# Kernel optimization log

Measured on AMD Instinct MI355X. Metric: run time of the kernel, lower is better.

Reference implementation:

```python
import jax, jax.numpy as jnp
import numpy as np

B, S, T, D = 32, 128, 65536, 768
VOCAB, N_SEC, N_TEMP, N_NEG, MAX_SENT, N_TS = 30522, 6, 3, 2, 128, 512
LN_EPS = 1e-5


def setup_inputs() -> dict:
    key = jax.random.key(0)
    ks = jax.random.split(key, 16)
    return {
        "token_ids": jax.random.randint(ks[0], (T,), 0, VOCAB),
        "segment_ids": jnp.sort(jax.random.randint(ks[1], (T,), 0, B * S)),
        "section_ids": jax.random.randint(ks[2], (B, S), 0, N_SEC),
        "temporality_ids": jax.random.randint(ks[3], (B, S), 0, N_TEMP),
        "negation_ids": jax.random.randint(ks[4], (B, S), 0, N_NEG),
        "position_ids": jax.random.randint(ks[5], (B, S), 0, MAX_SENT),
        "timestamp_ids": jax.random.randint(ks[6], (B, S), 0, N_TS),
        "token_table": jax.random.normal(ks[7], (VOCAB, D), jnp.float32),
        "section_table": jax.random.normal(ks[8], (N_SEC, D), jnp.float32),
        "temporality_table": jax.random.normal(ks[9], (N_TEMP, D), jnp.float32),
        "negation_table": jax.random.normal(ks[10], (N_NEG, D), jnp.float32),
        "position_table": jax.random.normal(ks[11], (MAX_SENT, D), jnp.float32),
        "timestamp_table": jax.random.normal(ks[12], (N_TS, D), jnp.float32),
        "ln_gamma": jnp.ones((D,), jnp.float32),
        "ln_beta": jnp.zeros((D,), jnp.float32),
        "proj_w": jax.random.normal(ks[13], (D, D), jnp.float32) * (1.0 / np.sqrt(D)),
        "proj_b": jnp.zeros((D,), jnp.float32),
    }


def reference(token_ids, segment_ids, section_ids, temporality_ids, negation_ids,
              position_ids, timestamp_ids, token_table, section_table,
              temporality_table, negation_table, position_table, timestamp_table,
              ln_gamma, ln_beta, proj_w, proj_b):
    # ragged per-sentence token-embedding mean pool (segment mean over B*S slots)
    tok = token_table[token_ids]                                  # [T, D]
    sums = jax.ops.segment_sum(tok, segment_ids, num_segments=B * S)
    cnt = jax.ops.segment_sum(jnp.ones((T,), tok.dtype), segment_ids,
                              num_segments=B * S)
    base = (sums / jnp.maximum(cnt, 1.0)[:, None]).reshape(B, S, D)
    # multi-embedding sum
    enriched = (base
                + section_table[section_ids]
                + temporality_table[temporality_ids]
                + negation_table[negation_ids]
                + position_table[position_ids]
                + timestamp_table[timestamp_ids])                 # [B, S, D]
    # LayerNorm + Linear
    mu = enriched.mean(-1, keepdims=True)
    var = jnp.mean(jnp.square(enriched - mu), axis=-1, keepdims=True)
    normed = (enriched - mu) * jax.lax.rsqrt(var + LN_EPS) * ln_gamma + ln_beta
    tokens = jnp.einsum('bsd,ed->bse', normed, proj_w) + proj_b   # [B, S, D]
    padding_mask = jnp.zeros((B, S), dtype=bool)                  # all sentences valid
    return tokens, padding_mask
```

## Files before the change

kernel.cpp:

```cpp
#include <hip/hip_runtime.h>
#include <stdint.h>

#define Tn 65536
#define Dn 768
#define NSEG 4096

typedef __bf16 bf16;
typedef __bf16 bf16x8 __attribute__((ext_vector_type(8)));
typedef float f32x4 __attribute__((ext_vector_type(4)));

__device__ inline void f4add(float4& a, const float4& v) {
  a.x += v.x; a.y += v.y; a.z += v.z; a.w += v.w;
}

__global__ __launch_bounds__(256) void k_prep(
    const float* __restrict__ w, bf16* __restrict__ wb,
    float* __restrict__ mask_out,
    const int* __restrict__ seg, int* __restrict__ starts)
{
  const int b = blockIdx.x;
  if (b < 576) {
    const int i = b * 256 + threadIdx.x;
    const float4 v = ((const float4*)w)[i];
    alignas(8) bf16 o[4] = {(bf16)v.x, (bf16)v.y, (bf16)v.z, (bf16)v.w};
    ((ushort4*)wb)[i] = *(ushort4*)o;
  } else if (b < 592) {
    mask_out[(b - 576) * 256 + threadIdx.x] = 0.0f;
  } else {
    const int t = (b - 592) * 256 + threadIdx.x;
    const int s = seg[t];
    const int sp = (t == 0) ? -1 : seg[t - 1];
    for (int k = sp + 1; k <= s; ++k) starts[k] = t;
    if (t == Tn - 1)
      for (int k = s + 1; k <= NSEG; ++k) starts[k] = Tn;
  }
}

__global__ void k_pool_ln(
    const int* __restrict__ token_ids, const int* __restrict__ starts,
    const int* __restrict__ section_ids, const int* __restrict__ temporality_ids,
    const int* __restrict__ negation_ids, const int* __restrict__ position_ids,
    const int* __restrict__ timestamp_ids,
    const float* __restrict__ token_table, const float* __restrict__ section_table,
    const float* __restrict__ temporality_table, const float* __restrict__ negation_table,
    const float* __restrict__ position_table, const float* __restrict__ timestamp_table,
    const float* __restrict__ gamma, const float* __restrict__ beta,
    bf16* __restrict__ out_normed)
{
  const int n = blockIdx.x;
  const int lane = threadIdx.x;
  const int start = starts[n];
  const int end   = starts[n + 1];
  const float scale = 1.0f / fmaxf((float)(end - start), 1.0f);

  const float4* tt = (const float4*)token_table;

  const float4* e1 = (const float4*)(section_table     + (size_t)section_ids[n]     * Dn);
  const float4* e2 = (const float4*)(temporality_table + (size_t)temporality_ids[n] * Dn);
  const float4* e3 = (const float4*)(negation_table    + (size_t)negation_ids[n]    * Dn);
  const float4* e4 = (const float4*)(position_table    + (size_t)position_ids[n]    * Dn);
  const float4* e5 = (const float4*)(timestamp_table   + (size_t)timestamp_ids[n]   * Dn);
  float4 en[3];
  #pragma unroll
  for (int j = 0; j < 3; ++j) {
    const int d = j * 64 + lane;
    float4 q = e1[d];
    f4add(q, e2[d]); f4add(q, e3[d]); f4add(q, e4[d]); f4add(q, e5[d]);
    en[j] = q;
  }

  float4 acc[3];
  #pragma unroll
  for (int j = 0; j < 3; ++j) acc[j] = make_float4(0.f, 0.f, 0.f, 0.f);

  int t = start;
  int ids[8];
  #pragma unroll
  for (int u = 0; u < 8; ++u)
    ids[u] = token_ids[(t + u < Tn) ? t + u : Tn - 1];

  while (t + 8 <= end) {
    float4 L[8][3];
    #pragma unroll
    for (int u = 0; u < 8; ++u) {
      const float4* r = tt + (size_t)ids[u] * 192;
      #pragma unroll
      for (int j = 0; j < 3; ++j) L[u][j] = r[j * 64 + lane];
    }
    t += 8;
    #pragma unroll
    for (int u = 0; u < 8; ++u)
      ids[u] = token_ids[(t + u < Tn) ? t + u : Tn - 1];
    #pragma unroll
    for (int j = 0; j < 3; ++j) {
      f4add(L[0][j], L[1][j]); f4add(L[2][j], L[3][j]);
      f4add(L[4][j], L[5][j]); f4add(L[6][j], L[7][j]);
      f4add(L[0][j], L[2][j]); f4add(L[4][j], L[6][j]);
      f4add(L[0][j], L[4][j]); f4add(acc[j], L[0][j]);
    }
  }
  for (int u = 0; t < end; ++t, ++u) {
    const float4* r = tt + (size_t)ids[u] * 192;
    #pragma unroll
    for (int j = 0; j < 3; ++j) f4add(acc[j], r[j * 64 + lane]);
  }

  float4 e[3];
  #pragma unroll
  for (int j = 0; j < 3; ++j) {
    e[j].x = acc[j].x * scale + en[j].x;
    e[j].y = acc[j].y * scale + en[j].y;
    e[j].z = acc[j].z * scale + en[j].z;
    e[j].w = acc[j].w * scale + en[j].w;
  }

  float s = 0.f;
  #pragma unroll
  for (int j = 0; j < 3; ++j) s += e[j].x + e[j].y + e[j].z + e[j].w;
  #pragma unroll
  for (int o = 32; o > 0; o >>= 1) s += __shfl_xor(s, o, 64);
  const float mu = s * (1.0f / 768.0f);

  float v = 0.f;
  #pragma unroll
  for (int j = 0; j < 3; ++j) {
    e[j].x -= mu; e[j].y -= mu; e[j].z -= mu; e[j].w -= mu;
    v += e[j].x * e[j].x + e[j].y * e[j].y + e[j].z * e[j].z + e[j].w * e[j].w;
  }
  #pragma unroll
  for (int o = 32; o > 0; o >>= 1) v += __shfl_xor(v, o, 64);
  const float inv = rsqrtf(v * (1.0f / 768.0f) + 1e-5f);

  #pragma unroll
  for (int j = 0; j < 3; ++j) {
    const int d = j * 64 + lane;
    const float4 g = ((const float4*)gamma)[d];
    const float4 b = ((const float4*)beta)[d];
    alignas(8) bf16 o[4];
    o[0] = (bf16)(e[j].x * inv * g.x + b.x);
    o[1] = (bf16)(e[j].y * inv * g.y + b.y);
    o[2] = (bf16)(e[j].z * inv * g.z + b.z);
    o[3] = (bf16)(e[j].w * inv * g.w + b.w);
    *(ushort4*)(out_normed + (size_t)n * Dn + 4 * d) = *(ushort4*)o;
  }
}

__global__ __launch_bounds__(256) void k_gemm(
    const bf16* __restrict__ A, const bf16* __restrict__ W,
    const float* __restrict__ bias, float* __restrict__ out)
{
  __shared__ bf16 As[64 * 32];
  __shared__ bf16 Bs[128 * 32];
  const int tid  = threadIdx.x;
  const int lane = tid & 63;
  const int w    = tid >> 6;
  const int m0 = blockIdx.y * 64;
  const int n0 = blockIdx.x * 128;
  const int wm = (w >> 1) * 32;
  const int wn = (w & 1) * 64;

  f32x4 acc[2][4];
  #pragma unroll
  for (int i = 0; i < 2; ++i)
    #pragma unroll
    for (int j = 0; j < 4; ++j) acc[i][j] = (f32x4){0.f, 0.f, 0.f, 0.f};

  const int fr = tid >> 2;
  const int fc = (tid & 3) * 8;
  const bf16* agp = A + (size_t)(m0 + fr) * 768 + fc;
  const bf16* bgp = W + (size_t)(n0 + fr) * 768 + fc;

  for (int kt = 0; kt < 24; ++kt) {
    __syncthreads();
    __builtin_amdgcn_global_load_lds(
        (const __attribute__((address_space(1))) void*)(agp + kt * 32),
        (__attribute__((address_space(3))) void*)(As + tid * 8), 16, 0, 0);
    #pragma unroll
    for (int it = 0; it < 2; ++it) {
      const int f = it * 256 + tid;
      __builtin_amdgcn_global_load_lds(
          (const __attribute__((address_space(1))) void*)(bgp + (size_t)it * 64 * 768 + kt * 32),
          (__attribute__((address_space(3))) void*)(Bs + f * 8), 16, 0, 0);
    }
    __syncthreads();

    bf16x8 af[2], bfr[4];
    #pragma unroll
    for (int i = 0; i < 2; ++i)
      af[i] = *(const bf16x8*)(As + (wm + i * 16 + (lane & 15)) * 32 + (lane >> 4) * 8);
    #pragma unroll
    for (int j = 0; j < 4; ++j)
      bfr[j] = *(const bf16x8*)(Bs + (wn + j * 16 + (lane & 15)) * 32 + (lane >> 4) * 8);

    #pragma unroll
    for (int i = 0; i < 2; ++i)
      #pragma unroll
      for (int j = 0; j < 4; ++j)
        acc[i][j] = __builtin_amdgcn_mfma_f32_16x16x32_bf16(af[i], bfr[j], acc[i][j], 0, 0, 0);
  }

  float bvals[4];
  #pragma unroll
  for (int j = 0; j < 4; ++j) bvals[j] = bias[n0 + wn + j * 16 + (lane & 15)];
  const int r0 = (lane >> 4) * 4;
  #pragma unroll
  for (int i = 0; i < 2; ++i) {
    #pragma unroll
    for (int r = 0; r < 4; ++r) {
      const int gm = m0 + wm + i * 16 + r0 + r;
      float* orow = out + (size_t)gm * 768 + n0 + wn;
      #pragma unroll
      for (int j = 0; j < 4; ++j)
        orow[j * 16 + (lane & 15)] = acc[i][j][r] + bvals[j];
    }
  }
}

extern "C" void kernel_launch(void* const* d_in, const int* in_sizes, int n_in,
                              void* d_out, int out_size, void* d_ws, size_t ws_size,
                              hipStream_t stream) {
  const int* token_ids       = (const int*)d_in[0];
  const int* segment_ids     = (const int*)d_in[1];
  const int* section_ids     = (const int*)d_in[2];
  const int* temporality_ids = (const int*)d_in[3];
  const int* negation_ids    = (const int*)d_in[4];
  const int* position_ids    = (const int*)d_in[5];
  const int* timestamp_ids   = (const int*)d_in[6];
  const float* token_table       = (const float*)d_in[7];
  const float* section_table     = (const float*)d_in[8];
  const float* temporality_table = (const float*)d_in[9];
  const float* negation_table    = (const float*)d_in[10];
  const float* position_table    = (const float*)d_in[11];
  const float* timestamp_table   = (const float*)d_in[12];
  const float* ln_gamma = (const float*)d_in[13];
  const float* ln_beta  = (const float*)d_in[14];
  const float* proj_w   = (const float*)d_in[15];
  const float* proj_b   = (const float*)d_in[16];

  float* out = (float*)d_out;
  bf16* wsW = (bf16*)d_ws;
  bf16* wsN = wsW + (size_t)Dn * Dn;
  int*  wsS = (int*)((char*)d_ws + (size_t)(Dn * Dn + NSEG * Dn) * 2);

  k_prep<<<848, 256, 0, stream>>>(proj_w, wsW, out + (size_t)NSEG * Dn,
                                  segment_ids, wsS);
  k_pool_ln<<<NSEG, 64, 0, stream>>>(token_ids, wsS, section_ids,
      temporality_ids, negation_ids, position_ids, timestamp_ids,
      token_table, section_table, temporality_table, negation_table,
      position_table, timestamp_table, ln_gamma, ln_beta, wsN);
  k_gemm<<<dim3(6, 64), 256, 0, stream>>>(wsN, wsW, proj_b, out);
}
```

Before: 202.8 us.

## Fuse prep into pooling kernel using per-segment binary search for bounds

Removes the separate prep kernel by folding the weight bf16 conversion and mask zeroing into extra blocks of the pooling kernel. Each segment block now finds its start and end with a 16-step binary search over segment_ids instead of reading a precomputed starts array. Token-row gathers use nontemporal loads, and the unroll drops from 8 to 6 with a launch-bounds occupancy hint. This saves a kernel launch and its dependency, at the cost of extra serialized global reads per block for the search.

```diff
diff --git a/kernel.cpp b/kernel.cpp
--- a/kernel.cpp
+++ b/kernel.cpp
@@ -9,35 +9,12 @@
 typedef __bf16 bf16x8 __attribute__((ext_vector_type(8)));
 typedef float f32x4 __attribute__((ext_vector_type(4)));
 
-__device__ inline void f4add(float4& a, const float4& v) {
-  a.x += v.x; a.y += v.y; a.z += v.z; a.w += v.w;
-}
-
-__global__ __launch_bounds__(256) void k_prep(
-    const float* __restrict__ w, bf16* __restrict__ wb,
-    float* __restrict__ mask_out,
-    const int* __restrict__ seg, int* __restrict__ starts)
-{
-  const int b = blockIdx.x;
-  if (b < 576) {
-    const int i = b * 256 + threadIdx.x;
-    const float4 v = ((const float4*)w)[i];
-    alignas(8) bf16 o[4] = {(bf16)v.x, (bf16)v.y, (bf16)v.z, (bf16)v.w};
-    ((ushort4*)wb)[i] = *(ushort4*)o;
-  } else if (b < 592) {
-    mask_out[(b - 576) * 256 + threadIdx.x] = 0.0f;
-  } else {
-    const int t = (b - 592) * 256 + threadIdx.x;
-    const int s = seg[t];
-    const int sp = (t == 0) ? -1 : seg[t - 1];
-    for (int k = sp + 1; k <= s; ++k) starts[k] = t;
-    if (t == Tn - 1)
-      for (int k = s + 1; k <= NSEG; ++k) starts[k] = Tn;
-  }
-}
-
-__global__ void k_pool_ln(
-    const int* __restrict__ token_ids, const int* __restrict__ starts,
+__device__ inline f32x4 ntload(const f32x4* p) {
+  return __builtin_nontemporal_load(p);
+}
+
+__global__ __launch_bounds__(64, 4) void k_fused(
+    const int* __restrict__ token_ids, const int* __restrict__ seg,
     const int* __restrict__ section_ids, const int* __restrict__ temporality_ids,
     const int* __restrict__ negation_ids, const int* __restrict__ position_ids,
     const int* __restrict__ timestamp_ids,
@@ -45,78 +22,98 @@
     const float* __restrict__ temporality_table, const float* __restrict__ negation_table,
     const float* __restrict__ position_table, const float* __restrict__ timestamp_table,
     const float* __restrict__ gamma, const float* __restrict__ beta,
-    bf16* __restrict__ out_normed)
+    bf16* __restrict__ out_normed,
+    const float* __restrict__ w, bf16* __restrict__ wb,
+    float* __restrict__ mask_out)
 {
-  const int n = blockIdx.x;
+  const int b = blockIdx.x;
   const int lane = threadIdx.x;
-  const int start = starts[n];
-  const int end   = starts[n + 1];
+
+  if (b >= NSEG) {
+    if (b < NSEG + 2304) {
+      const int i = (b - NSEG) * 64 + lane;
+      const float4 v = ((const float4*)w)[i];
+      alignas(8) bf16 o[4] = {(bf16)v.x, (bf16)v.y, (bf16)v.z, (bf16)v.w};
+      ((ushort4*)wb)[i] = *(ushort4*)o;
+    } else {
+      const int i = (b - (NSEG + 2304)) * 64 + lane;
+      ((float4*)mask_out)[i] = make_float4(0.f, 0.f, 0.f, 0.f);
+    }
+    return;
+  }
+
+  const int n = b;
+  int lo1 = 0, hi1 = Tn, lo2 = 0, hi2 = Tn;
+  #pragma unroll 1
+  for (int it = 0; it < 16; ++it) {
+    const int m1 = (lo1 + hi1) >> 1;
+    const int m2 = (lo2 + hi2) >> 1;
+    const int v1 = seg[m1];
+    const int v2 = seg[m2];
+    if (v1 < n)     lo1 = m1 + 1; else hi1 = m1;
+    if (v2 < n + 1) lo2 = m2 + 1; else hi2 = m2;
+  }
+  const int start = lo1, end = lo2;
   const float scale = 1.0f / fmaxf((float)(end - start), 1.0f);
 
-  const float4* tt = (const float4*)token_table;
-
-  const float4* e1 = (const float4*)(section_table     + (size_t)section_ids[n]     * Dn);
-  const float4* e2 = (const float4*)(temporality_table + (size_t)temporality_ids[n] * Dn);
-  const float4* e3 = (const float4*)(negation_table    + (size_t)negation_ids[n]    * Dn);
-  const float4* e4 = (const float4*)(position_table    + (size_t)position_ids[n]    * Dn);
-  const float4* e5 = (const float4*)(timestamp_table   + (size_t)timestamp_ids[n]   * Dn);
-  float4 en[3];
+  const f32x4* tt = (const f32x4*)token_table;
+
+  const f32x4* e1 = (const f32x4*)(section_table     + (size_t)section_ids[n]     * Dn);
+  const f32x4* e2 = (const f32x4*)(temporality_table + (size_t)temporality_ids[n] * Dn);
+  const f32x4* e3 = (const f32x4*)(negation_table    + (size_t)negation_ids[n]    * Dn);
+  const f32x4* e4 = (const f32x4*)(position_table    + (size_t)position_ids[n]    * Dn);
+  const f32x4* e5 = (const f32x4*)(timestamp_table   + (size_t)timestamp_ids[n]   * Dn);
+  f32x4 en[3];
   #pragma unroll
   for (int j = 0; j < 3; ++j) {
     const int d = j * 64 + lane;
-    float4 q = e1[d];
-    f4add(q, e2[d]); f4add(q, e3[d]); f4add(q, e4[d]); f4add(q, e5[d]);
-    en[j] = q;
-  }
-
-  float4 acc[3];
-  #pragma unroll
-  for (int j = 0; j < 3; ++j) acc[j] = make_float4(0.f, 0.f, 0.f, 0.f);
+    en[j] = e1[d] + e2[d] + e3[d] + e4[d] + e5[d];
+  }
+
+  f32x4 acc[3];
+  #pragma unroll
+  for (int j = 0; j < 3; ++j) acc[j] = (f32x4){0.f, 0.f, 0.f, 0.f};
 
   int t = start;
-  int ids[8];
-  #pragma unroll
-  for (int u = 0; u < 8; ++u)
+  int ids[6];
+  #pragma unroll
+  for (int u = 0; u < 6; ++u)
     ids[u] = token_ids[(t + u < Tn) ? t + u : Tn - 1];
 
-  while (t + 8 <= end) {
-    float4 L[8][3];
-    #pragma unroll
-    for (int u = 0; u < 8; ++u) {
-      const float4* r = tt + (size_t)ids[u] * 192;
-      #pragma unroll
-      for (int j = 0; j < 3; ++j) L[u][j] = r[j * 64 + lane];
-    }
-    t += 8;
-    #pragma unroll
-    for (int u = 0; u < 8; ++u)
+  while (t + 6 <= end) {
+    f32x4 L[6][3];
+    #pragma unroll
+    for (int u = 0; u < 6; ++u) {
+      const f32x4* r = tt + (size_t)ids[u] * 192;
+      #pragma unroll
+      for (int j = 0; j < 3; ++j) L[u][j] = ntload(r + j * 64 + lane);
+    }
+    t += 6;
+    #pragma unroll
+    for (int u = 0; u < 6; ++u)
       ids[u] = token_ids[(t + u < Tn) ? t + u : Tn - 1];
     #pragma unroll
     for (int j = 0; j < 3; ++j) {
-      f4add(L[0][j], L[1][j]); f4add(L[2][j], L[3][j]);
-      f4add(L[4][j], L[5][j]); f4add(L[6][j], L[7][j]);
-      f4add(L[0][j], L[2][j]); f4add(L[4][j], L[6][j]);
-      f4add(L[0][j], L[4][j]); f4add(acc[j], L[0][j]);
-    }
-  }
-  for (int u = 0; t < end; ++t, ++u) {
-    const float4* r = tt + (size_t)ids[u] * 192;
-    #pragma unroll
-    for (int j = 0; j < 3; ++j) f4add(acc[j], r[j * 64 + lane]);
-  }
-
-  float4 e[3];
-  #pragma unroll
-  for (int j = 0; j < 3; ++j) {
-    e[j].x = acc[j].x * scale + en[j].x;
-    e[j].y = acc[j].y * scale + en[j].y;
-    e[j].z = acc[j].z * scale + en[j].z;
-    e[j].w = acc[j].w * scale + en[j].w;
-  }
+      L[0][j] += L[1][j]; L[2][j] += L[3][j]; L[4][j] += L[5][j];
+      acc[j] += (L[0][j] + L[2][j]) + L[4][j];
+    }
+  }
+  #pragma unroll
+  for (int u = 0; u < 5; ++u) {
+    if (t + u < end) {
+      const f32x4* r = tt + (size_t)ids[u] * 192;
+      #pragma unroll
+      for (int j = 0; j < 3; ++j) acc[j] += ntload(r + j * 64 + lane);
+    }
+  }
+
+  f32x4 e[3];
+  #pragma unroll
+  for (int j = 0; j < 3; ++j) e[j] = acc[j] * scale + en[j];
 
   float s = 0.f;
   #pragma unroll
-  for (int j = 0; j < 3; ++j) s += e[j].x + e[j].y + e[j].z + e[j].w;
+  for (int j = 0; j < 3; ++j) s += e[j][0] + e[j][1] + e[j][2] + e[j][3];
   #pragma unroll
   for (int o = 32; o > 0; o >>= 1) s += __shfl_xor(s, o, 64);
   const float mu = s * (1.0f / 768.0f);
@@ -124,8 +121,8 @@
   float v = 0.f;
   #pragma unroll
   for (int j = 0; j < 3; ++j) {
-    e[j].x -= mu; e[j].y -= mu; e[j].z -= mu; e[j].w -= mu;
-    v += e[j].x * e[j].x + e[j].y * e[j].y + e[j].z * e[j].z + e[j].w * e[j].w;
+    e[j] -= mu;
+    v += e[j][0]*e[j][0] + e[j][1]*e[j][1] + e[j][2]*e[j][2] + e[j][3]*e[j][3];
   }
   #pragma unroll
   for (int o = 32; o > 0; o >>= 1) v += __shfl_xor(v, o, 64);
@@ -134,13 +131,10 @@
   #pragma unroll
   for (int j = 0; j < 3; ++j) {
     const int d = j * 64 + lane;
-    const float4 g = ((const float4*)gamma)[d];
-    const float4 b = ((const float4*)beta)[d];
-    alignas(8) bf16 o[4];
-    o[0] = (bf16)(e[j].x * inv * g.x + b.x);
-    o[1] = (bf16)(e[j].y * inv * g.y + b.y);
-    o[2] = (bf16)(e[j].z * inv * g.z + b.z);
-    o[3] = (bf16)(e[j].w * inv * g.w + b.w);
+    const f32x4 g = ((const f32x4*)gamma)[d];
+    const f32x4 bb = ((const f32x4*)beta)[d];
+    const f32x4 r = e[j] * inv * g + bb;
+    alignas(8) bf16 o[4] = {(bf16)r[0], (bf16)r[1], (bf16)r[2], (bf16)r[3]};
     *(ushort4*)(out_normed + (size_t)n * Dn + 4 * d) = *(ushort4*)o;
   }
 }
@@ -240,13 +234,11 @@
   float* out = (float*)d_out;
   bf16* wsW = (bf16*)d_ws;
   bf16* wsN = wsW + (size_t)Dn * Dn;
-  int*  wsS = (int*)((char*)d_ws + (size_t)(Dn * Dn + NSEG * Dn) * 2);
-
-  k_prep<<<848, 256, 0, stream>>>(proj_w, wsW, out + (size_t)NSEG * Dn,
-                                  segment_ids, wsS);
-  k_pool_ln<<<NSEG, 64, 0, stream>>>(token_ids, wsS, section_ids,
-      temporality_ids, negation_ids, position_ids, timestamp_ids,
+
+  k_fused<<<NSEG + 2304 + 16, 64, 0, stream>>>(token_ids, segment_ids,
+      section_ids, temporality_ids, negation_ids, position_ids, timestamp_ids,
       token_table, section_table, temporality_table, negation_table,
-      position_table, timestamp_table, ln_gamma, ln_beta, wsN);
+      position_table, timestamp_table, ln_gamma, ln_beta, wsN,
+      proj_w, wsW, out + (size_t)NSEG * Dn);
   k_gemm<<<dim3(6, 64), 256, 0, stream>>>(wsN, wsW, proj_b, out);
 }
```

Result: slower. 212.3 us (+4.7%).
